# Kernel optimization log

Hardware: AMD Instinct MI355X
Metric: run time of the kernel (lower is better)

Reference implementation:

```python
import jax, jax.numpy as jnp
import numpy as np

B, N, VDIM = 64, 256, 2048
LRDIM, EMBED = 64, 1024


def setup_inputs() -> dict:
    key = jax.random.key(0)
    ks = jax.random.split(key, 12)
    s = 1.0 / np.sqrt(VDIM)
    return {
        "Vmat": jax.random.normal(ks[0], (B, N, VDIM), dtype=jnp.float32),
        # weight-normed linear_U1: W = g * v / ||v||_row, bias b
        "U1_v": jax.random.normal(ks[1], (LRDIM, VDIM), dtype=jnp.float32) * s,
        "U1_g": jax.random.uniform(ks[2], (LRDIM,), dtype=jnp.float32, minval=0.5, maxval=1.5),
        "U1_b": jax.random.normal(ks[3], (LRDIM,), dtype=jnp.float32) * s,
        "U2_v": jax.random.normal(ks[4], (LRDIM, VDIM), dtype=jnp.float32) * s,
        "U2_g": jax.random.uniform(ks[5], (LRDIM,), dtype=jnp.float32, minval=0.5, maxval=1.5),
        "U2_b": jax.random.normal(ks[6], (LRDIM,), dtype=jnp.float32) * s,
        # final projection + BatchNorm1d affine params
        "W_lin": jax.random.normal(ks[7], (EMBED, VDIM), dtype=jnp.float32) * s,
        "b_lin": jax.random.normal(ks[8], (EMBED,), dtype=jnp.float32) * s,
        "bn_gamma": jnp.ones((EMBED,), dtype=jnp.float32),
        "bn_beta": jnp.zeros((EMBED,), dtype=jnp.float32),
    }


def _weight_norm(v, g):
    # torch weight_norm with dim=0: per output row
    return v * (g / jnp.linalg.norm(v, axis=1))[:, None]


def reference(Vmat, U1_v, U1_g, U1_b, U2_v, U2_g, U2_b, W_lin, b_lin, bn_gamma, bn_beta):
    # forward(Vmat, t_method='uncorr', model_num=6) -> UnCorrVmat_Detail path
    W1 = _weight_norm(U1_v, U1_g)
    W2 = _weight_norm(U2_v, U2_g)
    right = jax.nn.relu(jnp.einsum('bnv,kv->bnk', Vmat, W1) + U1_b)   # [B,N,LR]
    left = jax.nn.relu(jnp.einsum('bnv,kv->bnk', Vmat, W2) + U2_b)    # [B,N,LR]
    uncorr = jnp.einsum('bnk,bmk->bnm', left, right)                   # [B,N,N]
    # vectorized per-batch diag rsqrt normalization
    d = jax.lax.rsqrt(jnp.einsum('bii->bi', uncorr) + 1e-6)            # [B,N]
    uncorr = d[:, None, :] * uncorr * d[:, :, None]
    uncorr = 1.0 + jnp.eye(Vmat.shape[1], dtype=Vmat.dtype) - uncorr
    feats = jnp.mean(jnp.einsum('bnm,bmv->bnv', uncorr, Vmat), axis=1)  # [B,VDIM]
    # linear + BatchNorm1d (training mode: biased batch stats)
    x = feats @ W_lin.T + b_lin                                        # [B,EMBED]
    mu = jnp.mean(x, axis=0)
    var = jnp.mean(jnp.square(x - mu), axis=0)
    return bn_gamma * (x - mu) * jax.lax.rsqrt(var + 1e-5) + bn_beta
```

## Files before the change

kernel.cpp:

```cpp
#include <hip/hip_runtime.h>

#define B_ 64
#define N_ 256
#define V_ 2048
#define E_ 1024
#define MROWS 16384

typedef __bf16 bf16_t;
typedef bf16_t bf16x8 __attribute__((ext_vector_type(8)));
typedef float f32x4 __attribute__((ext_vector_type(4)));

#define OFF_S   0
#define OFF_LR  16384
#define OFF_FT  2113536
#define OFF_WB  2244608

__device__ __forceinline__ void gload_lds16(const bf16_t* g, bf16_t* l) {
    __builtin_amdgcn_global_load_lds((const __attribute__((address_space(1))) void*)g,
                                     (__attribute__((address_space(3))) void*)l, 16, 0, 0);
}

__global__ void kprep(const float* __restrict__ U1v, const float* __restrict__ U1g,
                      const float* __restrict__ U2v, const float* __restrict__ U2g,
                      bf16_t* __restrict__ Wb) {
    __shared__ float red[256];
    __shared__ float sc;
    const int r = blockIdx.x;
    const float* v = (r < 64) ? (U1v + (size_t)r * V_) : (U2v + (size_t)(r - 64) * V_);
    float ss = 0.f;
    for (int i = threadIdx.x; i < V_; i += 256) { float x = v[i]; ss += x * x; }
    red[threadIdx.x] = ss;
    __syncthreads();
    for (int o = 128; o > 0; o >>= 1) {
        if (threadIdx.x < (unsigned)o) red[threadIdx.x] += red[threadIdx.x + o];
        __syncthreads();
    }
    if (threadIdx.x == 0) {
        float g = (r < 64) ? U1g[r] : U2g[r - 64];
        sc = g * rsqrtf(red[0]);
    }
    __syncthreads();
    const float s = sc;
    const int k = threadIdx.x * 8;
    float4 f0 = *(const float4*)(v + k);
    float4 f1 = *(const float4*)(v + k + 4);
    bf16x8 o;
    o[0] = (bf16_t)(f0.x * s); o[1] = (bf16_t)(f0.y * s);
    o[2] = (bf16_t)(f0.z * s); o[3] = (bf16_t)(f0.w * s);
    o[4] = (bf16_t)(f1.x * s); o[5] = (bf16_t)(f1.y * s);
    o[6] = (bf16_t)(f1.z * s); o[7] = (bf16_t)(f1.w * s);
    *(bf16x8*)(Wb + (size_t)r * V_ + k) = o;
}

#define BK 64
__global__ __launch_bounds__(256) void gemm_lr(
    const float* __restrict__ V, const bf16_t* __restrict__ Wb,
    const float* __restrict__ U1b, const float* __restrict__ U2b,
    float* __restrict__ LR) {
    __shared__ bf16_t As[32 * BK];
    __shared__ bf16_t Bs[128 * BK];
    const int t = threadIdx.x;
    const int m0 = blockIdx.x * 32;
    const int wv = t >> 6, lane = t & 63;
    const int lm = lane & 15, lq = lane >> 4;
    const int n0w = wv * 32;

    const int arow = t >> 3, au = t & 7;
    const float* aptr = V + (size_t)(m0 + arow) * V_ + au * 8;
    bf16_t* adst = &As[arow * BK + ((au ^ (arow & 7)) * 8)];

    const int rloc = lane >> 3;
    const int uu = (lane & 7) ^ rloc;
    const bf16_t* bgbase = Wb + (size_t)(wv * 8 + rloc) * V_ + uu * 8;

    f32x4 acc[2][2];
#pragma unroll
    for (int i = 0; i < 2; ++i)
#pragma unroll
        for (int j = 0; j < 2; ++j) acc[i][j] = (f32x4){0.f, 0.f, 0.f, 0.f};

#pragma unroll
    for (int q = 0; q < 4; ++q)
        gload_lds16(bgbase + (size_t)q * 32 * V_, &Bs[(q * 32 + wv * 8) * BK]);
    float4 ap0 = *(const float4*)(aptr);
    float4 ap1 = *(const float4*)(aptr + 4);

    for (int k0 = 0; k0 < V_; k0 += BK) {
        bf16x8 av;
        av[0] = (bf16_t)ap0.x; av[1] = (bf16_t)ap0.y; av[2] = (bf16_t)ap0.z; av[3] = (bf16_t)ap0.w;
        av[4] = (bf16_t)ap1.x; av[5] = (bf16_t)ap1.y; av[6] = (bf16_t)ap1.z; av[7] = (bf16_t)ap1.w;
        *(bf16x8*)adst = av;
        __syncthreads();

        bf16x8 af[2][2], bfr[2][2];
#pragma unroll
        for (int i = 0; i < 2; ++i)
#pragma unroll
            for (int kf = 0; kf < 2; ++kf)
                af[i][kf] = *(bf16x8*)&As[(i * 16 + lm) * BK + (((kf * 4 + lq) ^ (lm & 7)) * 8)];
#pragma unroll
        for (int j = 0; j < 2; ++j)
#pragma unroll
            for (int kf = 0; kf < 2; ++kf)
                bfr[j][kf] = *(bf16x8*)&Bs[(n0w + j * 16 + lm) * BK + (((kf * 4 + lq) ^ (lm & 7)) * 8)];

        if (k0 + BK < V_) {
            ap0 = *(const float4*)(aptr + k0 + BK);
            ap1 = *(const float4*)(aptr + k0 + BK + 4);
        }
#pragma unroll
        for (int i = 0; i < 2; ++i)
#pragma unroll
            for (int j = 0; j < 2; ++j) {
                acc[i][j] = __builtin_amdgcn_mfma_f32_16x16x32_bf16(af[i][0], bfr[j][0], acc[i][j], 0, 0, 0);
                acc[i][j] = __builtin_amdgcn_mfma_f32_16x16x32_bf16(af[i][1], bfr[j][1], acc[i][j], 0, 0, 0);
            }
        __syncthreads();
        if (k0 + BK < V_) {
#pragma unroll
            for (int q = 0; q < 4; ++q)
                gload_lds16(bgbase + (size_t)q * 32 * V_ + (k0 + BK), &Bs[(q * 32 + wv * 8) * BK]);
        }
    }
#pragma unroll
    for (int j = 0; j < 2; ++j) {
        const int n = n0w + j * 16 + lm;
        const float bi = (n < 64) ? U1b[n] : U2b[n - 64];
#pragma unroll
        for (int i = 0; i < 2; ++i)
#pragma unroll
            for (int r = 0; r < 4; ++r) {
                const int m = m0 + i * 16 + lq * 4 + r;
                LR[(size_t)m * 128 + n] = fmaxf(acc[i][j][r] + bi, 0.f);
            }
    }
}

__global__ __launch_bounds__(256) void kds(const float* __restrict__ LR, float* __restrict__ s) {
    __shared__ float dl[256];
    __shared__ float red[4][64];
    __shared__ float lbar[64];
    const int b = blockIdx.x, t = threadIdx.x;
    const float* Lb = LR + (size_t)b * N_ * 128;
    const float* row = Lb + (size_t)t * 128;
    float dd = 0.f;
#pragma unroll
    for (int k = 0; k < 64; k += 4) {
        float4 l = *(const float4*)(row + k);
        float4 r = *(const float4*)(row + 64 + k);
        dd += l.x * r.x + l.y * r.y + l.z * r.z + l.w * r.w;
    }
    const float dv = rsqrtf(dd + 1e-6f);
    dl[t] = dv;
    __syncthreads();
    const int k = t & 63, g = t >> 6;
    float acc = 0.f;
    for (int n = g; n < N_; n += 4)
        acc += dl[n] * Lb[(size_t)n * 128 + 64 + k];
    red[g][k] = acc;
    __syncthreads();
    if (t < 64) lbar[t] = red[0][t] + red[1][t] + red[2][t] + red[3][t];
    __syncthreads();
    float a2 = 0.f;
#pragma unroll 8
    for (int kk = 0; kk < 64; ++kk) a2 += lbar[kk] * row[kk];
    s[b * N_ + t] = ((float)(N_ + 1) - dv * a2) * (1.0f / (float)N_);
}

__global__ __launch_bounds__(256) void kfeats(const float* __restrict__ Vmat,
                                              const float* __restrict__ s,
                                              float* __restrict__ featsT) {
    const int b = blockIdx.x >> 3, vc = (blockIdx.x >> 2) & 1, mc = blockIdx.x & 3;
    __shared__ float sl[64];
    const int t = threadIdx.x;
    if (t < 64) sl[t] = s[b * N_ + mc * 64 + t];
    __syncthreads();
    const int v = vc * 1024 + t * 4;
    const float* base = Vmat + (size_t)b * N_ * V_ + (size_t)mc * 64 * V_ + v;
    float4 a = {0.f, 0.f, 0.f, 0.f};
    for (int m = 0; m < 64; m += 8) {
        float4 x[8];
#pragma unroll
        for (int u = 0; u < 8; ++u) x[u] = *(const float4*)(base + (size_t)(m + u) * V_);
#pragma unroll
        for (int u = 0; u < 8; ++u) {
            float sv = sl[m + u];
            a.x += sv * x[u].x; a.y += sv * x[u].y;
            a.z += sv * x[u].z; a.w += sv * x[u].w;
        }
    }
    atomicAdd(&featsT[(size_t)(v + 0) * 64 + b], a.x);
    atomicAdd(&featsT[(size_t)(v + 1) * 64 + b], a.y);
    atomicAdd(&featsT[(size_t)(v + 2) * 64 + b], a.z);
    atomicAdd(&featsT[(size_t)(v + 3) * 64 + b], a.w);
}

__global__ __launch_bounds__(256) void klinbn(const float* __restrict__ featsT,
                                              const float* __restrict__ Wl,
                                              const float* __restrict__ gamma,
                                              const float* __restrict__ beta,
                                              float* __restrict__ out) {
    __shared__ float red[4][4][64];
    const int e0 = blockIdx.x * 4;
    const int t = threadIdx.x, b = t & 63, g = t >> 6;
    const float* w0 = Wl + (size_t)(e0 + 0) * V_ + g * 512;
    const float* w1 = Wl + (size_t)(e0 + 1) * V_ + g * 512;
    const float* w2 = Wl + (size_t)(e0 + 2) * V_ + g * 512;
    const float* w3 = Wl + (size_t)(e0 + 3) * V_ + g * 512;
    const float* f = featsT + (size_t)g * 512 * 64 + b;
    float a0 = 0.f, a1 = 0.f, a2 = 0.f, a3 = 0.f;
#pragma unroll 4
    for (int k = 0; k < 512; ++k) {
        float fv = f[(size_t)k * 64];
        a0 += fv * w0[k]; a1 += fv * w1[k]; a2 += fv * w2[k]; a3 += fv * w3[k];
    }
    red[g][0][b] = a0; red[g][1][b] = a1; red[g][2][b] = a2; red[g][3][b] = a3;
    __syncthreads();
    const int e = t >> 6;
    float v = red[0][e][b] + red[1][e][b] + red[2][e][b] + red[3][e][b];
    float sum = v;
#pragma unroll
    for (int o = 1; o < 64; o <<= 1) sum += __shfl_xor(sum, o, 64);
    float mu = sum * (1.f / 64.f);
    float dvv = v - mu;
    float q = dvv * dvv;
#pragma unroll
    for (int o = 1; o < 64; o <<= 1) q += __shfl_xor(q, o, 64);
    float inv = rsqrtf(q * (1.f / 64.f) + 1e-5f);
    float res = gamma[e0 + e] * dvv * inv + beta[e0 + e];
    __syncthreads();
    red[0][e][b] = res;
    __syncthreads();
    const int b2 = t >> 2, j = t & 3;
    out[(size_t)b2 * E_ + e0 + j] = red[0][j][b2];
}

extern "C" void kernel_launch(void* const* d_in, const int* in_sizes, int n_in,
                              void* d_out, int out_size, void* d_ws, size_t ws_size,
                              hipStream_t stream) {
    const float* Vmat = (const float*)d_in[0];
    const float* U1v  = (const float*)d_in[1];
    const float* U1g  = (const float*)d_in[2];
    const float* U1b  = (const float*)d_in[3];
    const float* U2v  = (const float*)d_in[4];
    const float* U2g  = (const float*)d_in[5];
    const float* U2b  = (const float*)d_in[6];
    const float* Wl   = (const float*)d_in[7];
    const float* gam  = (const float*)d_in[9];
    const float* bet  = (const float*)d_in[10];

    float*  ws     = (float*)d_ws;
    float*  s      = ws + OFF_S;
    float*  LR     = ws + OFF_LR;
    float*  featsT = ws + OFF_FT;
    bf16_t* Wb     = (bf16_t*)(ws + OFF_WB);

    hipMemsetAsync(featsT, 0, (size_t)V_ * B_ * sizeof(float), stream);
    kprep  <<<128, 256, 0, stream>>>(U1v, U1g, U2v, U2g, Wb);
    gemm_lr<<<MROWS / 32, 256, 0, stream>>>(Vmat, Wb, U1b, U2b, LR);
    kds    <<<B_, 256, 0, stream>>>(LR, s);
    kfeats <<<B_ * 8, 256, 0, stream>>>(Vmat, s, featsT);
    klinbn <<<E_ / 4, 256, 0, stream>>>(featsT, Wl, gam, bet, (float*)d_out);
}
```

Measured before the change: 323.6 us.

## Load GEMM operands directly into registers, fold featsT zeroing into kprep

gemm_lr no longer stages tiles in LDS. Each wave now loads its A (fp32 V, converted to bf16) and B (bf16 weights) fragments straight from global memory into MFMA registers, with only an occasional barrier to keep the waves roughly in step. This removes the LDS round trip and the per-iteration block synchronisation. The cost is that the four waves redundantly load the same A rows, and the global accesses are less coalesced, so more work falls on L1/L2. Separately, the hipMemsetAsync of featsT is replaced by zero stores inside kprep (128 blocks × 256 threads × 4 floats covers the 64×2048 buffer), which saves one launch.

```diff
diff --git a/kernel.cpp b/kernel.cpp
--- a/kernel.cpp
+++ b/kernel.cpp
@@ -15,14 +15,13 @@
 #define OFF_FT  2113536
 #define OFF_WB  2244608
 
-__device__ __forceinline__ void gload_lds16(const bf16_t* g, bf16_t* l) {
-    __builtin_amdgcn_global_load_lds((const __attribute__((address_space(1))) void*)g,
-                                     (__attribute__((address_space(3))) void*)l, 16, 0, 0);
-}
-
 __global__ void kprep(const float* __restrict__ U1v, const float* __restrict__ U1g,
                       const float* __restrict__ U2v, const float* __restrict__ U2g,
-                      bf16_t* __restrict__ Wb) {
+                      bf16_t* __restrict__ Wb, float* __restrict__ featsT) {
+    {
+        float4 z = {0.f, 0.f, 0.f, 0.f};
+        *(float4*)&featsT[(size_t)(blockIdx.x * 256 + threadIdx.x) * 4] = z;
+    }
     __shared__ float red[256];
     __shared__ float sc;
     const int r = blockIdx.x;
@@ -52,26 +51,20 @@
     *(bf16x8*)(Wb + (size_t)r * V_ + k) = o;
 }
 
-#define BK 64
 __global__ __launch_bounds__(256) void gemm_lr(
     const float* __restrict__ V, const bf16_t* __restrict__ Wb,
     const float* __restrict__ U1b, const float* __restrict__ U2b,
     float* __restrict__ LR) {
-    __shared__ bf16_t As[32 * BK];
-    __shared__ bf16_t Bs[128 * BK];
     const int t = threadIdx.x;
     const int m0 = blockIdx.x * 32;
     const int wv = t >> 6, lane = t & 63;
     const int lm = lane & 15, lq = lane >> 4;
     const int n0w = wv * 32;
 
-    const int arow = t >> 3, au = t & 7;
-    const float* aptr = V + (size_t)(m0 + arow) * V_ + au * 8;
-    bf16_t* adst = &As[arow * BK + ((au ^ (arow & 7)) * 8)];
-
-    const int rloc = lane >> 3;
-    const int uu = (lane & 7) ^ rloc;
-    const bf16_t* bgbase = Wb + (size_t)(wv * 8 + rloc) * V_ + uu * 8;
+    const float*  a0p = V  + (size_t)(m0 + lm) * V_ + lq * 8;
+    const float*  a1p = a0p + (size_t)16 * V_;
+    const bf16_t* b0p = Wb + (size_t)(n0w + lm) * V_ + lq * 8;
+    const bf16_t* b1p = b0p + (size_t)16 * V_;
 
     f32x4 acc[2][2];
 #pragma unroll
@@ -79,48 +72,27 @@
 #pragma unroll
         for (int j = 0; j < 2; ++j) acc[i][j] = (f32x4){0.f, 0.f, 0.f, 0.f};
 
-#pragma unroll
-    for (int q = 0; q < 4; ++q)
-        gload_lds16(bgbase + (size_t)q * 32 * V_, &Bs[(q * 32 + wv * 8) * BK]);
-    float4 ap0 = *(const float4*)(aptr);
-    float4 ap1 = *(const float4*)(aptr + 4);
-
-    for (int k0 = 0; k0 < V_; k0 += BK) {
-        bf16x8 av;
-        av[0] = (bf16_t)ap0.x; av[1] = (bf16_t)ap0.y; av[2] = (bf16_t)ap0.z; av[3] = (bf16_t)ap0.w;
-        av[4] = (bf16_t)ap1.x; av[5] = (bf16_t)ap1.y; av[6] = (bf16_t)ap1.z; av[7] = (bf16_t)ap1.w;
-        *(bf16x8*)adst = av;
-        __syncthreads();
-
-        bf16x8 af[2][2], bfr[2][2];
-#pragma unroll
-        for (int i = 0; i < 2; ++i)
-#pragma unroll
-            for (int kf = 0; kf < 2; ++kf)
-                af[i][kf] = *(bf16x8*)&As[(i * 16 + lm) * BK + (((kf * 4 + lq) ^ (lm & 7)) * 8)];
-#pragma unroll
-        for (int j = 0; j < 2; ++j)
-#pragma unroll
-            for (int kf = 0; kf < 2; ++kf)
-                bfr[j][kf] = *(bf16x8*)&Bs[(n0w + j * 16 + lm) * BK + (((kf * 4 + lq) ^ (lm & 7)) * 8)];
-
-        if (k0 + BK < V_) {
-            ap0 = *(const float4*)(aptr + k0 + BK);
-            ap1 = *(const float4*)(aptr + k0 + BK + 4);
+    for (int k0 = 0; k0 < V_; k0 += 64) {
+#pragma unroll
+        for (int h = 0; h < 2; ++h) {
+            const int k = k0 + h * 32;
+            float4 x00 = *(const float4*)(a0p + k);
+            float4 x01 = *(const float4*)(a0p + k + 4);
+            float4 x10 = *(const float4*)(a1p + k);
+            float4 x11 = *(const float4*)(a1p + k + 4);
+            bf16x8 bf0 = *(const bf16x8*)(b0p + k);
+            bf16x8 bf1 = *(const bf16x8*)(b1p + k);
+            bf16x8 af0, af1;
+            af0[0] = (bf16_t)x00.x; af0[1] = (bf16_t)x00.y; af0[2] = (bf16_t)x00.z; af0[3] = (bf16_t)x00.w;
+            af0[4] = (bf16_t)x01.x; af0[5] = (bf16_t)x01.y; af0[6] = (bf16_t)x01.z; af0[7] = (bf16_t)x01.w;
+            af1[0] = (bf16_t)x10.x; af1[1] = (bf16_t)x10.y; af1[2] = (bf16_t)x10.z; af1[3] = (bf16_t)x10.w;
+            af1[4] = (bf16_t)x11.x; af1[5] = (bf16_t)x11.y; af1[6] = (bf16_t)x11.z; af1[7] = (bf16_t)x11.w;
+            acc[0][0] = __builtin_amdgcn_mfma_f32_16x16x32_bf16(af0, bf0, acc[0][0], 0, 0, 0);
+            acc[0][1] = __builtin_amdgcn_mfma_f32_16x16x32_bf16(af0, bf1, acc[0][1], 0, 0, 0);
+            acc[1][0] = __builtin_amdgcn_mfma_f32_16x16x32_bf16(af1, bf0, acc[1][0], 0, 0, 0);
+            acc[1][1] = __builtin_amdgcn_mfma_f32_16x16x32_bf16(af1, bf1, acc[1][1], 0, 0, 0);
         }
-#pragma unroll
-        for (int i = 0; i < 2; ++i)
-#pragma unroll
-            for (int j = 0; j < 2; ++j) {
-                acc[i][j] = __builtin_amdgcn_mfma_f32_16x16x32_bf16(af[i][0], bfr[j][0], acc[i][j], 0, 0, 0);
-                acc[i][j] = __builtin_amdgcn_mfma_f32_16x16x32_bf16(af[i][1], bfr[j][1], acc[i][j], 0, 0, 0);
-            }
-        __syncthreads();
-        if (k0 + BK < V_) {
-#pragma unroll
-            for (int q = 0; q < 4; ++q)
-                gload_lds16(bgbase + (size_t)q * 32 * V_ + (k0 + BK), &Bs[(q * 32 + wv * 8) * BK]);
-        }
+        if (((k0 >> 6) & 7) == 7) __syncthreads();
     }
 #pragma unroll
     for (int j = 0; j < 2; ++j) {
@@ -255,8 +227,7 @@
     float*  featsT = ws + OFF_FT;
     bf16_t* Wb     = (bf16_t*)(ws + OFF_WB);
 
-    hipMemsetAsync(featsT, 0, (size_t)V_ * B_ * sizeof(float), stream);
-    kprep  <<<128, 256, 0, stream>>>(U1v, U1g, U2v, U2g, Wb);
+    kprep  <<<128, 256, 0, stream>>>(U1v, U1g, U2v, U2g, Wb, featsT);
     gemm_lr<<<MROWS / 32, 256, 0, stream>>>(Vmat, Wb, U1b, U2b, LR);
     kds    <<<B_, 256, 0, stream>>>(LR, s);
     kfeats <<<B_ * 8, 256, 0, stream>>>(Vmat, s, featsT);
```

New measurement: 358.3 us. 10.7% more time.

## Split low-rank GEMM along K into two halves and fold memset into prep

Applied to the files above, without the earlier changes.

The low-rank projection GEMM now launches a second grid dimension that splits the 2048-long reduction into two halves, each writing raw partial sums to its own buffer. Bias and ReLU are moved into the diagonal/scale kernel, which sums the two partials on read. This doubles the number of GEMM blocks (512 to 1024) to fill more compute units and shortens each block's serial K loop. The cost is extra LR traffic, since two partial buffers are written and read. The featsT memset is also folded into the prep kernel to remove one launch.

```diff
diff --git a/kernel.cpp b/kernel.cpp
--- a/kernel.cpp
+++ b/kernel.cpp
@@ -12,8 +12,9 @@
 
 #define OFF_S   0
 #define OFF_LR  16384
-#define OFF_FT  2113536
-#define OFF_WB  2244608
+#define OFF_FT  4210688
+#define OFF_WB  4341760
+#define LRHALF  2097152
 
 __device__ __forceinline__ void gload_lds16(const bf16_t* g, bf16_t* l) {
     __builtin_amdgcn_global_load_lds((const __attribute__((address_space(1))) void*)g,
@@ -22,7 +23,11 @@
 
 __global__ void kprep(const float* __restrict__ U1v, const float* __restrict__ U1g,
                       const float* __restrict__ U2v, const float* __restrict__ U2g,
-                      bf16_t* __restrict__ Wb) {
+                      bf16_t* __restrict__ Wb, float* __restrict__ featsT) {
+    {
+        float4 z = {0.f, 0.f, 0.f, 0.f};
+        *(float4*)&featsT[(size_t)(blockIdx.x * 256 + threadIdx.x) * 4] = z;
+    }
     __shared__ float red[256];
     __shared__ float sc;
     const int r = blockIdx.x;
@@ -53,25 +58,27 @@
 }
 
 #define BK 64
+#define KHALF 1024
 __global__ __launch_bounds__(256) void gemm_lr(
     const float* __restrict__ V, const bf16_t* __restrict__ Wb,
-    const float* __restrict__ U1b, const float* __restrict__ U2b,
-    float* __restrict__ LR) {
+    float* __restrict__ LRp) {
     __shared__ bf16_t As[32 * BK];
     __shared__ bf16_t Bs[128 * BK];
     const int t = threadIdx.x;
     const int m0 = blockIdx.x * 32;
+    const int kbase = blockIdx.y * KHALF;
+    float* LRh = LRp + (size_t)blockIdx.y * LRHALF;
     const int wv = t >> 6, lane = t & 63;
     const int lm = lane & 15, lq = lane >> 4;
     const int n0w = wv * 32;
 
     const int arow = t >> 3, au = t & 7;
-    const float* aptr = V + (size_t)(m0 + arow) * V_ + au * 8;
+    const float* aptr = V + (size_t)(m0 + arow) * V_ + kbase + au * 8;
     bf16_t* adst = &As[arow * BK + ((au ^ (arow & 7)) * 8)];
 
     const int rloc = lane >> 3;
     const int uu = (lane & 7) ^ rloc;
-    const bf16_t* bgbase = Wb + (size_t)(wv * 8 + rloc) * V_ + uu * 8;
+    const bf16_t* bgbase = Wb + (size_t)(wv * 8 + rloc) * V_ + kbase + uu * 8;
 
     f32x4 acc[2][2];
 #pragma unroll
@@ -85,7 +92,7 @@
     float4 ap0 = *(const float4*)(aptr);
     float4 ap1 = *(const float4*)(aptr + 4);
 
-    for (int k0 = 0; k0 < V_; k0 += BK) {
+    for (int k0 = 0; k0 < KHALF; k0 += BK) {
         bf16x8 av;
         av[0] = (bf16_t)ap0.x; av[1] = (bf16_t)ap0.y; av[2] = (bf16_t)ap0.z; av[3] = (bf16_t)ap0.w;
         av[4] = (bf16_t)ap1.x; av[5] = (bf16_t)ap1.y; av[6] = (bf16_t)ap1.z; av[7] = (bf16_t)ap1.w;
@@ -104,7 +111,7 @@
             for (int kf = 0; kf < 2; ++kf)
                 bfr[j][kf] = *(bf16x8*)&Bs[(n0w + j * 16 + lm) * BK + (((kf * 4 + lq) ^ (lm & 7)) * 8)];
 
-        if (k0 + BK < V_) {
+        if (k0 + BK < KHALF) {
             ap0 = *(const float4*)(aptr + k0 + BK);
             ap1 = *(const float4*)(aptr + k0 + BK + 4);
         }
@@ -116,7 +123,7 @@
                 acc[i][j] = __builtin_amdgcn_mfma_f32_16x16x32_bf16(af[i][1], bfr[j][1], acc[i][j], 0, 0, 0);
             }
         __syncthreads();
-        if (k0 + BK < V_) {
+        if (k0 + BK < KHALF) {
 #pragma unroll
             for (int q = 0; q < 4; ++q)
                 gload_lds16(bgbase + (size_t)q * 32 * V_ + (k0 + BK), &Bs[(q * 32 + wv * 8) * BK]);
@@ -125,45 +132,71 @@
 #pragma unroll
     for (int j = 0; j < 2; ++j) {
         const int n = n0w + j * 16 + lm;
-        const float bi = (n < 64) ? U1b[n] : U2b[n - 64];
 #pragma unroll
         for (int i = 0; i < 2; ++i)
 #pragma unroll
             for (int r = 0; r < 4; ++r) {
                 const int m = m0 + i * 16 + lq * 4 + r;
-                LR[(size_t)m * 128 + n] = fmaxf(acc[i][j][r] + bi, 0.f);
+                LRh[(size_t)m * 128 + n] = acc[i][j][r];
             }
     }
 }
 
-__global__ __launch_bounds__(256) void kds(const float* __restrict__ LR, float* __restrict__ s) {
+__global__ __launch_bounds__(256) void kds(const float* __restrict__ LRa,
+                                           const float* __restrict__ LRb,
+                                           const float* __restrict__ U1b,
+                                           const float* __restrict__ U2b,
+                                           float* __restrict__ s) {
     __shared__ float dl[256];
     __shared__ float red[4][64];
     __shared__ float lbar[64];
+    __shared__ float bias[128];
     const int b = blockIdx.x, t = threadIdx.x;
-    const float* Lb = LR + (size_t)b * N_ * 128;
-    const float* row = Lb + (size_t)t * 128;
+    if (t < 128) bias[t] = (t < 64) ? U1b[t] : U2b[t - 64];
+    __syncthreads();
+    const float* ra = LRa + (size_t)(b * N_ + t) * 128;
+    const float* rb = LRb + (size_t)(b * N_ + t) * 128;
     float dd = 0.f;
 #pragma unroll
     for (int k = 0; k < 64; k += 4) {
-        float4 l = *(const float4*)(row + k);
-        float4 r = *(const float4*)(row + 64 + k);
-        dd += l.x * r.x + l.y * r.y + l.z * r.z + l.w * r.w;
+        float4 xa = *(const float4*)(ra + k);
+        float4 xb = *(const float4*)(rb + k);
+        float4 ya = *(const float4*)(ra + 64 + k);
+        float4 yb = *(const float4*)(rb + 64 + k);
+        float r0 = fmaxf(xa.x + xb.x + bias[k + 0], 0.f);
+        float r1 = fmaxf(xa.y + xb.y + bias[k + 1], 0.f);
+        float r2 = fmaxf(xa.z + xb.z + bias[k + 2], 0.f);
+        float r3 = fmaxf(xa.w + xb.w + bias[k + 3], 0.f);
+        float l0 = fmaxf(ya.x + yb.x + bias[64 + k + 0], 0.f);
+        float l1 = fmaxf(ya.y + yb.y + bias[64 + k + 1], 0.f);
+        float l2 = fmaxf(ya.z + yb.z + bias[64 + k + 2], 0.f);
+        float l3 = fmaxf(ya.w + yb.w + bias[64 + k + 3], 0.f);
+        dd += r0 * l0 + r1 * l1 + r2 * l2 + r3 * l3;
     }
     const float dv = rsqrtf(dd + 1e-6f);
     dl[t] = dv;
     __syncthreads();
     const int k = t & 63, g = t >> 6;
+    const float bl = bias[64 + k];
     float acc = 0.f;
-    for (int n = g; n < N_; n += 4)
-        acc += dl[n] * Lb[(size_t)n * 128 + 64 + k];
+    for (int n = g; n < N_; n += 4) {
+        size_t idx = (size_t)(b * N_ + n) * 128 + 64 + k;
+        acc += dl[n] * fmaxf(LRa[idx] + LRb[idx] + bl, 0.f);
+    }
     red[g][k] = acc;
     __syncthreads();
     if (t < 64) lbar[t] = red[0][t] + red[1][t] + red[2][t] + red[3][t];
     __syncthreads();
     float a2 = 0.f;
-#pragma unroll 8
-    for (int kk = 0; kk < 64; ++kk) a2 += lbar[kk] * row[kk];
+#pragma unroll 4
+    for (int kk = 0; kk < 64; kk += 4) {
+        float4 xa = *(const float4*)(ra + kk);
+        float4 xb = *(const float4*)(rb + kk);
+        a2 += lbar[kk + 0] * fmaxf(xa.x + xb.x + bias[kk + 0], 0.f)
+            + lbar[kk + 1] * fmaxf(xa.y + xb.y + bias[kk + 1], 0.f)
+            + lbar[kk + 2] * fmaxf(xa.z + xb.z + bias[kk + 2], 0.f)
+            + lbar[kk + 3] * fmaxf(xa.w + xb.w + bias[kk + 3], 0.f);
+    }
     s[b * N_ + t] = ((float)(N_ + 1) - dv * a2) * (1.0f / (float)N_);
 }
 
@@ -251,14 +284,14 @@
 
     float*  ws     = (float*)d_ws;
     float*  s      = ws + OFF_S;
-    float*  LR     = ws + OFF_LR;
+    float*  LRa    = ws + OFF_LR;
+    float*  LRb    = ws + OFF_LR + LRHALF;
     float*  featsT = ws + OFF_FT;
     bf16_t* Wb     = (bf16_t*)(ws + OFF_WB);
 
-    hipMemsetAsync(featsT, 0, (size_t)V_ * B_ * sizeof(float), stream);
-    kprep  <<<128, 256, 0, stream>>>(U1v, U1g, U2v, U2g, Wb);
-    gemm_lr<<<MROWS / 32, 256, 0, stream>>>(Vmat, Wb, U1b, U2b, LR);
-    kds    <<<B_, 256, 0, stream>>>(LR, s);
+    kprep  <<<128, 256, 0, stream>>>(U1v, U1g, U2v, U2g, Wb, featsT);
+    gemm_lr<<<dim3(MROWS / 32, 2), 256, 0, stream>>>(Vmat, Wb, LRa);
+    kds    <<<B_, 256, 0, stream>>>(LRa, LRb, U1b, U2b, s);
     kfeats <<<B_ * 8, 256, 0, stream>>>(Vmat, s, featsT);
     klinbn <<<E_ / 4, 256, 0, stream>>>(featsT, Wl, gam, bet, (float*)d_out);
 }
```

After: 335.1 us. 3.6% more time.

## Register-prefetch two K-stages in LR GEMM and fold featsT zeroing into kprep

Applied to the files above, without the earlier changes.

The low-rank GEMM drops the async global-to-LDS loads for the weight tile. Both the A tile (fp32 Vmat) and the B tile (bf16 weights) are now prefetched into registers two 64-wide K-stages ahead and stored to LDS with an XOR swizzle. This is meant to hide global latency better, at the cost of more registers and extra VGPR-to-LDS store traffic. The separate memset of featsT is removed and done inside kprep, which saves one launch.

```diff
diff --git a/kernel.cpp b/kernel.cpp
--- a/kernel.cpp
+++ b/kernel.cpp
@@ -15,14 +15,13 @@
 #define OFF_FT  2113536
 #define OFF_WB  2244608
 
-__device__ __forceinline__ void gload_lds16(const bf16_t* g, bf16_t* l) {
-    __builtin_amdgcn_global_load_lds((const __attribute__((address_space(1))) void*)g,
-                                     (__attribute__((address_space(3))) void*)l, 16, 0, 0);
-}
-
 __global__ void kprep(const float* __restrict__ U1v, const float* __restrict__ U1g,
                       const float* __restrict__ U2v, const float* __restrict__ U2g,
-                      bf16_t* __restrict__ Wb) {
+                      bf16_t* __restrict__ Wb, float* __restrict__ featsT) {
+    {
+        float4 z = {0.f, 0.f, 0.f, 0.f};
+        *(float4*)&featsT[(size_t)(blockIdx.x * 256 + threadIdx.x) * 4] = z;
+    }
     __shared__ float red[256];
     __shared__ float sc;
     const int r = blockIdx.x;
@@ -65,13 +64,17 @@
     const int lm = lane & 15, lq = lane >> 4;
     const int n0w = wv * 32;
 
-    const int arow = t >> 3, au = t & 7;
-    const float* aptr = V + (size_t)(m0 + arow) * V_ + au * 8;
-    bf16_t* adst = &As[arow * BK + ((au ^ (arow & 7)) * 8)];
-
-    const int rloc = lane >> 3;
-    const int uu = (lane & 7) ^ rloc;
-    const bf16_t* bgbase = Wb + (size_t)(wv * 8 + rloc) * V_ + uu * 8;
+    const int ar = t >> 3, au = t & 7;
+    const float* aptr = V + (size_t)(m0 + ar) * V_ + au * 8;
+    bf16_t* adst = &As[ar * BK + ((au ^ (ar & 7)) * 8)];
+
+    const int br = t >> 1, bh = t & 1;
+    const bf16_t* bptr = Wb + (size_t)br * V_ + bh * 32;
+    bf16_t* bdst = &Bs[br * BK];
+    const int bperm0 = (bh * 4 + 0) ^ (br & 7);
+    const int bperm1 = (bh * 4 + 1) ^ (br & 7);
+    const int bperm2 = (bh * 4 + 2) ^ (br & 7);
+    const int bperm3 = (bh * 4 + 3) ^ (br & 7);
 
     f32x4 acc[2][2];
 #pragma unroll
@@ -79,47 +82,61 @@
 #pragma unroll
         for (int j = 0; j < 2; ++j) acc[i][j] = (f32x4){0.f, 0.f, 0.f, 0.f};
 
-#pragma unroll
-    for (int q = 0; q < 4; ++q)
-        gload_lds16(bgbase + (size_t)q * 32 * V_, &Bs[(q * 32 + wv * 8) * BK]);
-    float4 ap0 = *(const float4*)(aptr);
-    float4 ap1 = *(const float4*)(aptr + 4);
-
-    for (int k0 = 0; k0 < V_; k0 += BK) {
-        bf16x8 av;
-        av[0] = (bf16_t)ap0.x; av[1] = (bf16_t)ap0.y; av[2] = (bf16_t)ap0.z; av[3] = (bf16_t)ap0.w;
-        av[4] = (bf16_t)ap1.x; av[5] = (bf16_t)ap1.y; av[6] = (bf16_t)ap1.z; av[7] = (bf16_t)ap1.w;
-        *(bf16x8*)adst = av;
-        __syncthreads();
-
-        bf16x8 af[2][2], bfr[2][2];
-#pragma unroll
-        for (int i = 0; i < 2; ++i)
-#pragma unroll
-            for (int kf = 0; kf < 2; ++kf)
-                af[i][kf] = *(bf16x8*)&As[(i * 16 + lm) * BK + (((kf * 4 + lq) ^ (lm & 7)) * 8)];
-#pragma unroll
-        for (int j = 0; j < 2; ++j)
-#pragma unroll
-            for (int kf = 0; kf < 2; ++kf)
-                bfr[j][kf] = *(bf16x8*)&Bs[(n0w + j * 16 + lm) * BK + (((kf * 4 + lq) ^ (lm & 7)) * 8)];
-
-        if (k0 + BK < V_) {
-            ap0 = *(const float4*)(aptr + k0 + BK);
-            ap1 = *(const float4*)(aptr + k0 + BK + 4);
-        }
-#pragma unroll
-        for (int i = 0; i < 2; ++i)
-#pragma unroll
-            for (int j = 0; j < 2; ++j) {
-                acc[i][j] = __builtin_amdgcn_mfma_f32_16x16x32_bf16(af[i][0], bfr[j][0], acc[i][j], 0, 0, 0);
-                acc[i][j] = __builtin_amdgcn_mfma_f32_16x16x32_bf16(af[i][1], bfr[j][1], acc[i][j], 0, 0, 0);
+    float4 a0s[2], a1s[2];
+    uint4  bbs[2][4];
+#pragma unroll
+    for (int p = 0; p < 2; ++p) {
+        a0s[p] = *(const float4*)(aptr + p * 64);
+        a1s[p] = *(const float4*)(aptr + p * 64 + 4);
+#pragma unroll
+        for (int c = 0; c < 4; ++c)
+            bbs[p][c] = *(const uint4*)(bptr + p * 64 + c * 8);
+    }
+
+    for (int k0 = 0; k0 < V_; k0 += 128) {
+#pragma unroll
+        for (int pp = 0; pp < 2; ++pp) {
+            const int kc = k0 + pp * 64;
+            {
+                bf16x8 av;
+                av[0] = (bf16_t)a0s[pp].x; av[1] = (bf16_t)a0s[pp].y;
+                av[2] = (bf16_t)a0s[pp].z; av[3] = (bf16_t)a0s[pp].w;
+                av[4] = (bf16_t)a1s[pp].x; av[5] = (bf16_t)a1s[pp].y;
+                av[6] = (bf16_t)a1s[pp].z; av[7] = (bf16_t)a1s[pp].w;
+                *(bf16x8*)adst = av;
+                *(uint4*)(bdst + bperm0 * 8) = bbs[pp][0];
+                *(uint4*)(bdst + bperm1 * 8) = bbs[pp][1];
+                *(uint4*)(bdst + bperm2 * 8) = bbs[pp][2];
+                *(uint4*)(bdst + bperm3 * 8) = bbs[pp][3];
             }
-        __syncthreads();
-        if (k0 + BK < V_) {
-#pragma unroll
-            for (int q = 0; q < 4; ++q)
-                gload_lds16(bgbase + (size_t)q * 32 * V_ + (k0 + BK), &Bs[(q * 32 + wv * 8) * BK]);
+            if (kc + 128 < V_) {
+                a0s[pp] = *(const float4*)(aptr + kc + 128);
+                a1s[pp] = *(const float4*)(aptr + kc + 128 + 4);
+#pragma unroll
+                for (int c = 0; c < 4; ++c)
+                    bbs[pp][c] = *(const uint4*)(bptr + kc + 128 + c * 8);
+            }
+            __syncthreads();
+
+            bf16x8 af[2][2], bfr[2][2];
+#pragma unroll
+            for (int i = 0; i < 2; ++i)
+#pragma unroll
+                for (int kf = 0; kf < 2; ++kf)
+                    af[i][kf] = *(bf16x8*)&As[(i * 16 + lm) * BK + (((kf * 4 + lq) ^ (lm & 7)) * 8)];
+#pragma unroll
+            for (int j = 0; j < 2; ++j)
+#pragma unroll
+                for (int kf = 0; kf < 2; ++kf)
+                    bfr[j][kf] = *(bf16x8*)&Bs[(n0w + j * 16 + lm) * BK + (((kf * 4 + lq) ^ (lm & 7)) * 8)];
+#pragma unroll
+            for (int i = 0; i < 2; ++i)
+#pragma unroll
+                for (int j = 0; j < 2; ++j) {
+                    acc[i][j] = __builtin_amdgcn_mfma_f32_16x16x32_bf16(af[i][0], bfr[j][0], acc[i][j], 0, 0, 0);
+                    acc[i][j] = __builtin_amdgcn_mfma_f32_16x16x32_bf16(af[i][1], bfr[j][1], acc[i][j], 0, 0, 0);
+                }
+            __syncthreads();
         }
     }
 #pragma unroll
@@ -255,8 +272,7 @@
     float*  featsT = ws + OFF_FT;
     bf16_t* Wb     = (bf16_t*)(ws + OFF_WB);
 
-    hipMemsetAsync(featsT, 0, (size_t)V_ * B_ * sizeof(float), stream);
-    kprep  <<<128, 256, 0, stream>>>(U1v, U1g, U2v, U2g, Wb);
+    kprep  <<<128, 256, 0, stream>>>(U1v, U1g, U2v, U2g, Wb, featsT);
     gemm_lr<<<MROWS / 32, 256, 0, stream>>>(Vmat, Wb, U1b, U2b, LR);
     kds    <<<B_, 256, 0, stream>>>(LR, s);
     kfeats <<<B_ * 8, 256, 0, stream>>>(Vmat, s, featsT);
```

Result: slower. 396.7 us (+22.6%).
